# Kernel optimization log

Hardware: AMD Instinct MI355X
Metric: run time of the kernel (lower is better)

Reference implementation:

```python
import jax, jax.numpy as jnp
import numpy as np
import math

Ds = 2048
N = 16384
M = 1024


def setup_inputs() -> dict:
    key = jax.random.key(0)
    kD, kS, kW = jax.random.split(key, 3)
    D = jax.random.normal(kD, (N, Ds), dtype=jnp.float32)
    S = jax.random.normal(kS, (M, Ds), dtype=jnp.float32)
    W = jax.random.normal(kW, (Ds, Ds), dtype=jnp.float32) * 0.01  # init.normal std=0.01
    return {"D": D, "S": S, "W": W}


def reference(D, S, W):
    ds = D.shape[1]
    temperature = 1.0
    # cross-attention: [n, m]
    scores = (D @ S.T) / (math.sqrt(ds) * temperature)
    att_weight = jax.nn.softmax(scores, axis=1)
    att_S = att_weight @ S  # [n, Ds]
    # bilinear per row: logits[i] = D[i] . (W @ att_S[i])  -> fused einsum
    logits = jnp.einsum('nd,de,ne->n', D, W, att_S)
    log_prob = jnp.sum(jax.nn.log_sigmoid(logits))
    return log_prob
```

## Files before the change

kernel.cpp:

```cpp
#include <hip/hip_runtime.h>
#include <stdint.h>

typedef unsigned short u16;
typedef unsigned int u32;
typedef __attribute__((ext_vector_type(8))) short bf16x8;
typedef __attribute__((ext_vector_type(4))) float f32x4;

#define DS 2048
#define NROWS 16384
#define MS 1024
#define K2 2048

__device__ __forceinline__ u16 f2bf(float f) {
  u32 u = __float_as_uint(f);
  u32 r = (u + 0x7fffu + ((u >> 16) & 1u)) >> 16;
  return (u16)r;
}
__device__ __forceinline__ float bf2f(u16 h) {
  return __uint_as_float(((u32)h) << 16);
}

__global__ __launch_bounds__(256) void k_conv(const float* __restrict__ in,
                                              u16* __restrict__ out, int n4) {
  int i = blockIdx.x * blockDim.x + threadIdx.x;
  int stride = gridDim.x * blockDim.x;
  for (; i < n4; i += stride) {
    float4 v = ((const float4*)in)[i];
    ushort4 o;
    o.x = f2bf(v.x); o.y = f2bf(v.y); o.z = f2bf(v.z); o.w = f2bf(v.w);
    ((ushort4*)out)[i] = o;
  }
}

__global__ __launch_bounds__(256) void k_conv_S(const float* __restrict__ in,
                                                u16* __restrict__ Sbf,
                                                u16* __restrict__ Bt, int n4) {
  int i = blockIdx.x * blockDim.x + threadIdx.x;
  int stride = gridDim.x * blockDim.x;
  for (; i < n4; i += stride) {
    float4 v = ((const float4*)in)[i];
    ushort4 o;
    o.x = f2bf(v.x); o.y = f2bf(v.y); o.z = f2bf(v.z); o.w = f2bf(v.w);
    ((ushort4*)Sbf)[i] = o;
    int m = i >> 9;
    int c4 = i & 511;
    ((ushort4*)Bt)[(size_t)m * 1024 + c4] = o;
  }
}

__device__ __forceinline__ void gload16(const u16* g, u16* l) {
  __builtin_amdgcn_global_load_lds(
      (const __attribute__((address_space(1))) void*)g,
      (__attribute__((address_space(3))) void*)l, 16, 0, 0);
}

__global__ __launch_bounds__(256, 2) void k_gemm_bt64(const u16* __restrict__ A,
                                                      const u16* __restrict__ Bt,
                                                      u16* __restrict__ C, int ldc,
                                                      int K) {
  __shared__ u16 lsA[64 * 32];
  __shared__ u16 lsB[128 * 32];
  const int tid = threadIdx.x;
  const int wid = tid >> 6;
  const int lane = tid & 63;
  const int brow = blockIdx.y * 64;
  const int bcol = blockIdx.x * 128;
  const int wm = wid >> 1;
  const int wn = wid & 1;

  f32x4 acc[2][4];
#pragma unroll
  for (int i = 0; i < 2; ++i)
#pragma unroll
    for (int j = 0; j < 4; ++j) acc[i][j] = (f32x4){0.f, 0.f, 0.f, 0.f};

  const int srow = lane >> 2;
  const int skoct = (lane & 3) * 8;
  const u16* gA = A + (size_t)(brow + wid * 16 + srow) * K + skoct;
  const u16* gB = Bt + (size_t)(bcol + wid * 32 + srow) * K + skoct;
  u16* lA = &lsA[(wid * 16) * 32];
  u16* lB0 = &lsB[(wid * 32) * 32];
  u16* lB1 = &lsB[(wid * 32 + 16) * 32];
  const size_t row16 = (size_t)16 * K;

  const int arow = wm * 32 + (lane & 15);
  const int bcr = wn * 64 + (lane & 15);
  const int koff = (lane >> 4) * 8;

  for (int kt = 0; kt < K; kt += 32) {
    gload16(gA + kt, lA);
    gload16(gB + kt, lB0);
    gload16(gB + kt + row16, lB1);
    __syncthreads();
    bf16x8 af[2], bfr[4];
#pragma unroll
    for (int i = 0; i < 2; ++i) af[i] = *(const bf16x8*)&lsA[(arow + i * 16) * 32 + koff];
#pragma unroll
    for (int i = 0; i < 4; ++i) bfr[i] = *(const bf16x8*)&lsB[(bcr + i * 16) * 32 + koff];
#pragma unroll
    for (int mi = 0; mi < 2; ++mi)
#pragma unroll
      for (int ni = 0; ni < 4; ++ni)
        acc[mi][ni] = __builtin_amdgcn_mfma_f32_16x16x32_bf16(af[mi], bfr[ni],
                                                              acc[mi][ni], 0, 0, 0);
    __syncthreads();
  }

  const int crow0 = brow + wm * 32 + (lane >> 4) * 4;
  const int ccol0 = bcol + wn * 64 + (lane & 15);
#pragma unroll
  for (int mi = 0; mi < 2; ++mi)
#pragma unroll
    for (int ni = 0; ni < 4; ++ni)
#pragma unroll
      for (int r = 0; r < 4; ++r)
        C[(size_t)(crow0 + mi * 16 + r) * ldc + (ccol0 + ni * 16)] = f2bf(acc[mi][ni][r]);
}

#define SINV 0.022097086912079608f

#define DSR(d, a, IMM) \
  asm volatile("ds_read_b128 %0, %1 offset:%c2" : "=v"(d) : "v"(a), "n"(IMM))

#define RD_A0(k0, k1, dst)                              \
  DSR(dst[0][0], k0, 0);     DSR(dst[0][1], k1, 0);     \
  DSR(dst[1][0], k0, 2048);  DSR(dst[1][1], k1, 2048);  \
  DSR(dst[2][0], k0, 4096);  DSR(dst[2][1], k1, 4096);  \
  DSR(dst[3][0], k0, 6144);  DSR(dst[3][1], k1, 6144)
#define RD_A1(k0, k1, dst)                              \
  DSR(dst[0][0], k0, 16384); DSR(dst[0][1], k1, 16384); \
  DSR(dst[1][0], k0, 18432); DSR(dst[1][1], k1, 18432); \
  DSR(dst[2][0], k0, 20480); DSR(dst[2][1], k1, 20480); \
  DSR(dst[3][0], k0, 22528); DSR(dst[3][1], k1, 22528)
#define RD_B0(k0, k1, dst)                              \
  DSR(dst[0][0], k0, 0);     DSR(dst[0][1], k1, 0);     \
  DSR(dst[1][0], k0, 2048);  DSR(dst[1][1], k1, 2048)
#define RD_B1(k0, k1, dst)                              \
  DSR(dst[0][0], k0, 16384); DSR(dst[0][1], k1, 16384); \
  DSR(dst[1][0], k0, 18432); DSR(dst[1][1], k1, 18432)

#define MMAQ(AF, BQ, QM, QN)                                                       \
  do {                                                                             \
    _Pragma("unroll") for (int mi = 0; mi < 4; ++mi)                               \
        _Pragma("unroll") for (int ni = 0; ni < 2; ++ni) {                         \
      acc[QM][QN][mi][ni] = __builtin_amdgcn_mfma_f32_16x16x32_bf16(               \
          AF[mi][0], BQ[ni][0], acc[QM][QN][mi][ni], 0, 0, 0);                     \
      acc[QM][QN][mi][ni] = __builtin_amdgcn_mfma_f32_16x16x32_bf16(               \
          AF[mi][1], BQ[ni][1], acc[QM][QN][mi][ni], 0, 0, 0);                     \
    }                                                                              \
  } while (0)

#define LGKM(N)                                              \
  asm volatile("s_waitcnt lgkmcnt(" #N ")" ::: "memory");    \
  __builtin_amdgcn_sched_barrier(0)
#define VMW(N) asm volatile("s_waitcnt vmcnt(" #N ")" ::: "memory")
#define PRIO1() __builtin_amdgcn_s_setprio(1)
#define PRIO0() __builtin_amdgcn_s_setprio(0)
#define BAR() __builtin_amdgcn_s_barrier()

#define STGA(b, h, kt)                                                            \
  do {                                                                            \
    gload16(pA + (size_t)((h) * 128) * K2 + (kt),                                 \
            &lds[(b) * 32768 + (h) * 8192 + wid * 512]);                          \
    gload16(pA + (size_t)((h) * 128 + 64) * K2 + (kt),                            \
            &lds[(b) * 32768 + (h) * 8192 + 4096 + wid * 512]);                   \
  } while (0)
#define STGB(b, h, kt)                                                            \
  do {                                                                            \
    gload16(pB + (size_t)((h) * 128) * K2 + (kt),                                 \
            &lds[(b) * 32768 + 16384 + (h) * 8192 + wid * 512]);                  \
    gload16(pB + (size_t)((h) * 128 + 64) * K2 + (kt),                            \
            &lds[(b) * 32768 + 16384 + (h) * 8192 + 4096 + wid * 512]);           \
  } while (0)

__global__ __launch_bounds__(512, 2) void k_gemm8(const u16* __restrict__ A,
                                                  const u16* __restrict__ Bt,
                                                  float* __restrict__ Pnd) {
  extern __shared__ u16 lds[];
  const int tid = threadIdx.x;
  const int wid = tid >> 6;
  const int lane = tid & 63;
  const int bid = blockIdx.x;
  const int swz = (bid & 7) * 64 + (bid >> 3);
  const int by = swz >> 3, bx = swz & 7;
  const int brow = by * 256, bcol = bx * 256;
  const int wm = wid >> 2, wn = wid & 3;
  const int l15 = lane & 15, s0 = lane >> 4;

  const int tr = tid >> 3;
  const int scol = ((tid & 7) ^ (tr & 7)) << 3;
  const u16* pA = A + (size_t)(brow + tr) * K2 + scol;
  const u16* pB = Bt + (size_t)(bcol + tr) * K2 + scol;

  const u32 lb = (u32)(uintptr_t)(&lds[0]);
  const u32 xorp = ((u32)(s0 ^ (lane & 7))) << 4;
  const u32 aA00 = lb + ((u32)(wm * 64 + l15) << 7) + xorp;
  const u32 aA01 = aA00 ^ 64u;
  const u32 aA10 = aA00 + 65536u;
  const u32 aA11 = aA10 ^ 64u;
  const u32 aB00 = lb + 32768u + ((u32)(wn * 32 + l15) << 7) + xorp;
  const u32 aB01 = aB00 ^ 64u;
  const u32 aB10 = aB00 + 65536u;
  const u32 aB11 = aB10 ^ 64u;

  f32x4 acc[2][2][4][2];
#pragma unroll
  for (int a = 0; a < 2; ++a)
#pragma unroll
    for (int b = 0; b < 2; ++b)
#pragma unroll
      for (int c = 0; c < 4; ++c)
#pragma unroll
        for (int d = 0; d < 2; ++d) acc[a][b][c][d] = (f32x4){0.f, 0.f, 0.f, 0.f};

  bf16x8 afA[4][2], afB[4][2], bq0[2][2], bq1[2][2];

  STGA(0, 0, 0); STGB(0, 0, 0); STGB(0, 1, 0); STGA(0, 1, 0);
  STGA(1, 0, 64);
  VMW(2);
  BAR();
  RD_A0(aA00, aA01, afA);
  RD_B0(aB00, aB01, bq0);

  int kb = 0;
#pragma unroll 1
  for (int j = 0; j < 15; ++j, kb += 128) {
    STGB(1, 0, kb + 64);
    RD_B1(aB00, aB01, bq1);
    LGKM(4); PRIO1(); MMAQ(afA, bq0, 0, 0); PRIO0(); VMW(4); BAR();
    STGB(1, 1, kb + 64);
    RD_A1(aA00, aA01, afB);
    LGKM(8); PRIO1(); MMAQ(afA, bq1, 0, 1); PRIO0(); VMW(4); BAR();
    STGA(1, 1, kb + 64);
    LGKM(0); PRIO1(); MMAQ(afB, bq0, 1, 0); PRIO0(); VMW(4); BAR();
    STGA(0, 0, kb + 128);
    RD_A0(aA10, aA11, afA);
    RD_B0(aB10, aB11, bq0);
    LGKM(12); PRIO1(); MMAQ(afB, bq1, 1, 1); PRIO0(); VMW(4); BAR();
    STGB(0, 0, kb + 128);
    RD_B1(aB10, aB11, bq1);
    LGKM(4); PRIO1(); MMAQ(afA, bq0, 0, 0); PRIO0(); VMW(4); BAR();
    STGB(0, 1, kb + 128);
    RD_A1(aA10, aA11, afB);
    LGKM(8); PRIO1(); MMAQ(afA, bq1, 0, 1); PRIO0(); VMW(4); BAR();
    STGA(0, 1, kb + 128);
    LGKM(0); PRIO1(); MMAQ(afB, bq0, 1, 0); PRIO0(); VMW(4); BAR();
    STGA(1, 0, kb + 192);
    RD_A0(aA00, aA01, afA);
    RD_B0(aB00, aB01, bq0);
    LGKM(12); PRIO1(); MMAQ(afB, bq1, 1, 1); PRIO0(); VMW(4); BAR();
  }
  {
    STGB(1, 0, kb + 64);
    RD_B1(aB00, aB01, bq1);
    LGKM(4); PRIO1(); MMAQ(afA, bq0, 0, 0); PRIO0(); VMW(4); BAR();
    STGB(1, 1, kb + 64);
    RD_A1(aA00, aA01, afB);
    LGKM(8); PRIO1(); MMAQ(afA, bq1, 0, 1); PRIO0(); VMW(4); BAR();
    STGA(1, 1, kb + 64);
    LGKM(0); PRIO1(); MMAQ(afB, bq0, 1, 0); PRIO0(); VMW(4); BAR();
    RD_A0(aA10, aA11, afA);
    RD_B0(aB10, aB11, bq0);
    LGKM(12); PRIO1(); MMAQ(afB, bq1, 1, 1); PRIO0(); VMW(2); BAR();
    RD_B1(aB10, aB11, bq1);
    LGKM(4); PRIO1(); MMAQ(afA, bq0, 0, 0); PRIO0(); VMW(0); BAR();
    RD_A1(aA10, aA11, afB);
    LGKM(8); PRIO1(); MMAQ(afA, bq1, 0, 1); PRIO0();
    LGKM(0); PRIO1(); MMAQ(afB, bq0, 1, 0); PRIO0();
    MMAQ(afB, bq1, 1, 1);
  }

  __syncthreads();
  float* red = (float*)&lds[0];

#pragma unroll
  for (int qm = 0; qm < 2; ++qm)
#pragma unroll
    for (int mi = 0; mi < 4; ++mi)
#pragma unroll
      for (int r = 0; r < 4; ++r) {
        float num = 0.f, den = 0.f;
#pragma unroll
        for (int qn = 0; qn < 2; ++qn)
#pragma unroll
          for (int ni = 0; ni < 2; ++ni) {
            float v = acc[qm][qn][mi][ni][r];
            float g = __shfl_xor(v, 1);
            float e = __expf(v * SINV);
            num += e * g;
            den += e;
          }
        num += __shfl_xor(num, 2); den += __shfl_xor(den, 2);
        num += __shfl_xor(num, 4); den += __shfl_xor(den, 4);
        num += __shfl_xor(num, 8); den += __shfl_xor(den, 8);
        if (l15 == 0) {
          int slot = qm * 16 + mi * 4 + r;
          red[((wid * 32 + slot) * 4 + s0) * 2 + 0] = num;
          red[((wid * 32 + slot) * 4 + s0) * 2 + 1] = den;
        }
      }
  __syncthreads();
  {
    int rloc = tid >> 1, which = tid & 1;
    int qm = rloc >> 7, wmr = (rloc >> 6) & 1, mi = (rloc >> 4) & 3;
    int lg = (rloc >> 2) & 3, r = rloc & 3;
    int slot = qm * 16 + mi * 4 + r;
    float v = 0.f;
#pragma unroll
    for (int w2 = 0; w2 < 4; ++w2)
      v += red[(((wmr * 4 + w2) * 32 + slot) * 4 + lg) * 2 + which];
    Pnd[((size_t)(brow + rloc) * 8 + bx) * 2 + which] = v;
  }
}

__global__ __launch_bounds__(256) void k_rowfinal(const float* __restrict__ Pnd,
                                                  float* __restrict__ part) {
  int row = blockIdx.x * 256 + threadIdx.x;
  const float4* p = (const float4*)(Pnd + (size_t)row * 16);
  float num = 0.f, den = 0.f;
#pragma unroll
  for (int i = 0; i < 4; ++i) {
    float4 v = p[i];
    num += v.x + v.z;
    den += v.y + v.w;
  }
  float logit = num / den;
  float ls = (logit >= 0.f) ? -log1pf(__expf(-logit))
                            : (logit - log1pf(__expf(logit)));
  __shared__ float red[4];
#pragma unroll
  for (int off = 32; off > 0; off >>= 1) ls += __shfl_down(ls, off);
  if ((threadIdx.x & 63) == 0) red[threadIdx.x >> 6] = ls;
  __syncthreads();
  if (threadIdx.x == 0) part[blockIdx.x] = red[0] + red[1] + red[2] + red[3];
}

__global__ __launch_bounds__(64) void k_final64(const float* __restrict__ part,
                                                float* __restrict__ out) {
  float v = part[threadIdx.x];
#pragma unroll
  for (int off = 32; off > 0; off >>= 1) v += __shfl_down(v, off);
  if (threadIdx.x == 0) out[0] = v;
}

extern "C" void kernel_launch(void* const* d_in, const int* in_sizes, int n_in,
                              void* d_out, int out_size, void* d_ws, size_t ws_size,
                              hipStream_t stream) {
  const float* D = (const float*)d_in[0];
  const float* S = (const float*)d_in[1];
  const float* W = (const float*)d_in[2];

  char* w = (char*)d_ws;
  u16* Dbf = (u16*)w; w += (size_t)NROWS * DS * 2;
  u16* Bt = (u16*)w;  w += (size_t)DS * DS * 2;
  u16* Wbf = (u16*)w; w += (size_t)DS * DS * 2;
  u16* Sbf = (u16*)w; w += (size_t)MS * DS * 2;
  float* Pnd = (float*)w; w += (size_t)NROWS * 16 * 4;
  float* part = (float*)w;

  (void)hipFuncSetAttribute((const void*)k_gemm8,
                            hipFuncAttributeMaxDynamicSharedMemorySize, 131072);

  k_conv<<<1024, 256, 0, stream>>>(W, Wbf, DS * DS / 4);
  k_conv_S<<<512, 256, 0, stream>>>(S, Sbf, Bt, MS * DS / 4);
  k_conv<<<2048, 256, 0, stream>>>(D, Dbf, NROWS * DS / 4);

  k_gemm_bt64<<<dim3(DS / 128, MS / 64), 256, 0, stream>>>(
      Sbf, Wbf, Bt + DS, 2 * DS, DS);

  k_gemm8<<<512, 512, 131072, stream>>>(Dbf, Bt, Pnd);

  k_rowfinal<<<NROWS / 256, 256, 0, stream>>>(Pnd, part);
  k_final64<<<1, 64, 0, stream>>>(part, (float*)d_out);
}
```

Measured before the change: 188.7 us.

## Fuse conversions and S·W gemm into one pre-kernel loading fp32 directly

Replaces three conversion kernels and the small bf16 S×W gemm with a single launch. The first 256 blocks run the S×W gemm straight from fp32 inputs. They stage tiles into swizzled, double-buffered LDS with global_load_lds, convert to bf16 in registers with v_cvt_pk_bf16_f32, and issue MFMAs. The remaining blocks convert D and S to bf16. This removes the Wbf and Sbf intermediate buffers and several launches, and lets the gemm overlap with the D conversion. The cost is twice the LDS traffic per tile and a mixed-role grid.

```diff
diff --git a/kernel.cpp b/kernel.cpp
--- a/kernel.cpp
+++ b/kernel.cpp
@@ -5,6 +5,7 @@
 typedef unsigned int u32;
 typedef __attribute__((ext_vector_type(8))) short bf16x8;
 typedef __attribute__((ext_vector_type(4))) float f32x4;
+typedef __attribute__((ext_vector_type(4))) u32 u32x4;
 
 #define DS 2048
 #define NROWS 16384
@@ -16,37 +17,6 @@
   u32 r = (u + 0x7fffu + ((u >> 16) & 1u)) >> 16;
   return (u16)r;
 }
-__device__ __forceinline__ float bf2f(u16 h) {
-  return __uint_as_float(((u32)h) << 16);
-}
-
-__global__ __launch_bounds__(256) void k_conv(const float* __restrict__ in,
-                                              u16* __restrict__ out, int n4) {
-  int i = blockIdx.x * blockDim.x + threadIdx.x;
-  int stride = gridDim.x * blockDim.x;
-  for (; i < n4; i += stride) {
-    float4 v = ((const float4*)in)[i];
-    ushort4 o;
-    o.x = f2bf(v.x); o.y = f2bf(v.y); o.z = f2bf(v.z); o.w = f2bf(v.w);
-    ((ushort4*)out)[i] = o;
-  }
-}
-
-__global__ __launch_bounds__(256) void k_conv_S(const float* __restrict__ in,
-                                                u16* __restrict__ Sbf,
-                                                u16* __restrict__ Bt, int n4) {
-  int i = blockIdx.x * blockDim.x + threadIdx.x;
-  int stride = gridDim.x * blockDim.x;
-  for (; i < n4; i += stride) {
-    float4 v = ((const float4*)in)[i];
-    ushort4 o;
-    o.x = f2bf(v.x); o.y = f2bf(v.y); o.z = f2bf(v.z); o.w = f2bf(v.w);
-    ((ushort4*)Sbf)[i] = o;
-    int m = i >> 9;
-    int c4 = i & 511;
-    ((ushort4*)Bt)[(size_t)m * 1024 + c4] = o;
-  }
-}
 
 __device__ __forceinline__ void gload16(const u16* g, u16* l) {
   __builtin_amdgcn_global_load_lds(
@@ -54,19 +24,80 @@
       (__attribute__((address_space(3))) void*)l, 16, 0, 0);
 }
 
-__global__ __launch_bounds__(256, 2) void k_gemm_bt64(const u16* __restrict__ A,
-                                                      const u16* __restrict__ Bt,
-                                                      u16* __restrict__ C, int ldc,
-                                                      int K) {
-  __shared__ u16 lsA[64 * 32];
-  __shared__ u16 lsB[128 * 32];
+#define DSR(d, a, IMM) \
+  asm volatile("ds_read_b128 %0, %1 offset:%c2" : "=v"(d) : "v"(a), "n"(IMM))
+#define CVTPK(d, lo, hi) \
+  asm("v_cvt_pk_bf16_f32 %0, %1, %2" : "=v"(d) : "v"(lo), "v"(hi))
+#define LGKM(N)                                              \
+  asm volatile("s_waitcnt lgkmcnt(" #N ")" ::: "memory");    \
+  __builtin_amdgcn_sched_barrier(0)
+#define VMW(N) asm volatile("s_waitcnt vmcnt(" #N ")" ::: "memory")
+#define SB0() __builtin_amdgcn_sched_barrier(0)
+#define PRIO1() __builtin_amdgcn_s_setprio(1)
+#define PRIO0() __builtin_amdgcn_s_setprio(0)
+#define BAR() __builtin_amdgcn_s_barrier()
+
+#define CVT8(dst, lo, hi)                                         \
+  do {                                                            \
+    u32 _c0, _c1, _c2, _c3;                                       \
+    CVTPK(_c0, lo[0], lo[1]); CVTPK(_c1, lo[2], lo[3]);           \
+    CVTPK(_c2, hi[0], hi[1]); CVTPK(_c3, hi[2], hi[3]);           \
+    u32x4 _q = {_c0, _c1, _c2, _c3};                              \
+    dst = *(bf16x8*)&_q;                                          \
+  } while (0)
+
+__global__ __launch_bounds__(256) void k_pre(const float* __restrict__ D,
+                                             const float* __restrict__ S,
+                                             const float* __restrict__ W,
+                                             u16* __restrict__ Dbf,
+                                             u16* __restrict__ Bt) {
+  __shared__ float lsA[2][64 * 32];
+  __shared__ float lsB[2][128 * 32];
+  const int bid = blockIdx.x;
   const int tid = threadIdx.x;
-  const int wid = tid >> 6;
-  const int lane = tid & 63;
-  const int brow = blockIdx.y * 64;
-  const int bcol = blockIdx.x * 128;
-  const int wm = wid >> 1;
-  const int wn = wid & 1;
+
+  if (bid >= 256) {
+    if (bid < 2304) {
+      size_t i = (size_t)(bid - 256) * 256 + tid;
+#pragma unroll
+      for (int it = 0; it < 16; ++it, i += (size_t)2048 * 256) {
+        float4 v = ((const float4*)D)[i];
+        ushort4 o;
+        o.x = f2bf(v.x); o.y = f2bf(v.y); o.z = f2bf(v.z); o.w = f2bf(v.w);
+        ((ushort4*)Dbf)[i] = o;
+      }
+    } else {
+      size_t j = (size_t)(bid - 2304) * 256 + tid;
+#pragma unroll
+      for (int it = 0; it < 16; ++it, j += (size_t)128 * 256) {
+        float4 v = ((const float4*)S)[j];
+        ushort4 o;
+        o.x = f2bf(v.x); o.y = f2bf(v.y); o.z = f2bf(v.z); o.w = f2bf(v.w);
+        int m = (int)(j >> 9), c4 = (int)(j & 511);
+        ((ushort4*)Bt)[(size_t)m * 1024 + c4] = o;
+      }
+    }
+    return;
+  }
+
+  const int wid = tid >> 6, lane = tid & 63;
+  const int brow = (bid >> 4) * 64;
+  const int bcol = (bid & 15) * 128;
+  const int wm = wid >> 1, wn = wid & 1;
+  const int l15 = lane & 15, s0 = lane >> 4;
+
+  const int sr = tid >> 3;
+  const int soct = (tid & 7) ^ (sr & 7);
+  const float* gS = S + (size_t)(brow + sr) * 2048 + soct * 4;
+  const float* gW = W + (size_t)(bcol + sr) * 2048 + soct * 4;
+
+  const u32 lbA = (u32)(uintptr_t)&lsA[0][0];
+  const u32 lbB = (u32)(uintptr_t)&lsB[0][0];
+  const u32 swz = (u32)(((2 * s0) ^ (l15 & 7)) * 16);
+  const u32 aA = lbA + (u32)(wm * 32 + l15) * 128 + swz;
+  const u32 aAx = aA ^ 16u;
+  const u32 aB = lbB + (u32)(wn * 64 + l15) * 128 + swz;
+  const u32 aBx = aB ^ 16u;
 
   f32x4 acc[2][4];
 #pragma unroll
@@ -74,53 +105,67 @@
 #pragma unroll
     for (int j = 0; j < 4; ++j) acc[i][j] = (f32x4){0.f, 0.f, 0.f, 0.f};
 
-  const int srow = lane >> 2;
-  const int skoct = (lane & 3) * 8;
-  const u16* gA = A + (size_t)(brow + wid * 16 + srow) * K + skoct;
-  const u16* gB = Bt + (size_t)(bcol + wid * 32 + srow) * K + skoct;
-  u16* lA = &lsA[(wid * 16) * 32];
-  u16* lB0 = &lsB[(wid * 32) * 32];
-  u16* lB1 = &lsB[(wid * 32 + 16) * 32];
-  const size_t row16 = (size_t)16 * K;
-
-  const int arow = wm * 32 + (lane & 15);
-  const int bcr = wn * 64 + (lane & 15);
-  const int koff = (lane >> 4) * 8;
-
-  for (int kt = 0; kt < K; kt += 32) {
-    gload16(gA + kt, lA);
-    gload16(gB + kt, lB0);
-    gload16(gB + kt + row16, lB1);
-    __syncthreads();
+#define VSTG(b, kt)                                                              \
+  do {                                                                           \
+    gload16((const u16*)(gS + (kt)),             (u16*)(&lsA[b][0] + wid * 256)); \
+    gload16((const u16*)(gS + 32 * 2048 + (kt)), (u16*)(&lsA[b][1024] + wid * 256)); \
+    gload16((const u16*)(gW + (kt)),             (u16*)(&lsB[b][0] + wid * 256)); \
+    gload16((const u16*)(gW + 32 * 2048 + (kt)), (u16*)(&lsB[b][1024] + wid * 256)); \
+    gload16((const u16*)(gW + 64 * 2048 + (kt)), (u16*)(&lsB[b][2048] + wid * 256)); \
+    gload16((const u16*)(gW + 96 * 2048 + (kt)), (u16*)(&lsB[b][3072] + wid * 256)); \
+  } while (0)
+
+  VSTG(0, 0);
+#pragma unroll 1
+  for (int t = 0; t < 64; ++t) {
+    const int b = t & 1;
+    const u32 oA = (u32)(b * 8192), oB = (u32)(b * 16384);
+    if (t < 63) {
+      VSTG(b ^ 1, (t + 1) * 32);
+      VMW(6);
+    } else {
+      VMW(0);
+    }
+    BAR(); SB0();
+    f32x4 qa0, qa1, qa2, qa3;
+    f32x4 qb0, qb1, qb2, qb3, qb4, qb5, qb6, qb7;
+    DSR(qa0, aA + oA, 0);     DSR(qa1, aAx + oA, 0);
+    DSR(qa2, aA + oA, 2048);  DSR(qa3, aAx + oA, 2048);
+    DSR(qb0, aB + oB, 0);     DSR(qb1, aBx + oB, 0);
+    DSR(qb2, aB + oB, 2048);  DSR(qb3, aBx + oB, 2048);
+    DSR(qb4, aB + oB, 4096);  DSR(qb5, aBx + oB, 4096);
+    DSR(qb6, aB + oB, 6144);  DSR(qb7, aBx + oB, 6144);
+    LGKM(0);
     bf16x8 af[2], bfr[4];
-#pragma unroll
-    for (int i = 0; i < 2; ++i) af[i] = *(const bf16x8*)&lsA[(arow + i * 16) * 32 + koff];
-#pragma unroll
-    for (int i = 0; i < 4; ++i) bfr[i] = *(const bf16x8*)&lsB[(bcr + i * 16) * 32 + koff];
+    CVT8(af[0], qa0, qa1); CVT8(af[1], qa2, qa3);
+    CVT8(bfr[0], qb0, qb1); CVT8(bfr[1], qb2, qb3);
+    CVT8(bfr[2], qb4, qb5); CVT8(bfr[3], qb6, qb7);
+    PRIO1();
 #pragma unroll
     for (int mi = 0; mi < 2; ++mi)
 #pragma unroll
       for (int ni = 0; ni < 4; ++ni)
         acc[mi][ni] = __builtin_amdgcn_mfma_f32_16x16x32_bf16(af[mi], bfr[ni],
                                                               acc[mi][ni], 0, 0, 0);
-    __syncthreads();
-  }
-
-  const int crow0 = brow + wm * 32 + (lane >> 4) * 4;
-  const int ccol0 = bcol + wn * 64 + (lane & 15);
+    PRIO0(); SB0();
+    BAR();
+  }
+#undef VSTG
+
+  const int crow0 = brow + wm * 32 + s0 * 4;
+  const int ccol0 = bcol + wn * 64 + l15;
+  u16* C = Bt + 2048;
 #pragma unroll
   for (int mi = 0; mi < 2; ++mi)
 #pragma unroll
     for (int ni = 0; ni < 4; ++ni)
 #pragma unroll
       for (int r = 0; r < 4; ++r)
-        C[(size_t)(crow0 + mi * 16 + r) * ldc + (ccol0 + ni * 16)] = f2bf(acc[mi][ni][r]);
+        C[(size_t)(crow0 + mi * 16 + r) * 4096 + (ccol0 + ni * 16)] =
+            f2bf(acc[mi][ni][r]);
 }
 
 #define SINV 0.022097086912079608f
-
-#define DSR(d, a, IMM) \
-  asm volatile("ds_read_b128 %0, %1 offset:%c2" : "=v"(d) : "v"(a), "n"(IMM))
 
 #define RD_A0(k0, k1, dst)                              \
   DSR(dst[0][0], k0, 0);     DSR(dst[0][1], k1, 0);     \
@@ -149,14 +194,6 @@
           AF[mi][1], BQ[ni][1], acc[QM][QN][mi][ni], 0, 0, 0);                     \
     }                                                                              \
   } while (0)
-
-#define LGKM(N)                                              \
-  asm volatile("s_waitcnt lgkmcnt(" #N ")" ::: "memory");    \
-  __builtin_amdgcn_sched_barrier(0)
-#define VMW(N) asm volatile("s_waitcnt vmcnt(" #N ")" ::: "memory")
-#define PRIO1() __builtin_amdgcn_s_setprio(1)
-#define PRIO0() __builtin_amdgcn_s_setprio(0)
-#define BAR() __builtin_amdgcn_s_barrier()
 
 #define STGA(b, h, kt)                                                            \
   do {                                                                            \
@@ -353,20 +390,13 @@
   char* w = (char*)d_ws;
   u16* Dbf = (u16*)w; w += (size_t)NROWS * DS * 2;
   u16* Bt = (u16*)w;  w += (size_t)DS * DS * 2;
-  u16* Wbf = (u16*)w; w += (size_t)DS * DS * 2;
-  u16* Sbf = (u16*)w; w += (size_t)MS * DS * 2;
   float* Pnd = (float*)w; w += (size_t)NROWS * 16 * 4;
   float* part = (float*)w;
 
   (void)hipFuncSetAttribute((const void*)k_gemm8,
                             hipFuncAttributeMaxDynamicSharedMemorySize, 131072);
 
-  k_conv<<<1024, 256, 0, stream>>>(W, Wbf, DS * DS / 4);
-  k_conv_S<<<512, 256, 0, stream>>>(S, Sbf, Bt, MS * DS / 4);
-  k_conv<<<2048, 256, 0, stream>>>(D, Dbf, NROWS * DS / 4);
-
-  k_gemm_bt64<<<dim3(DS / 128, MS / 64), 256, 0, stream>>>(
-      Sbf, Wbf, Bt + DS, 2 * DS, DS);
+  k_pre<<<2432, 256, 0, stream>>>(D, S, W, Dbf, Bt);
 
   k_gemm8<<<512, 512, 131072, stream>>>(Dbf, Bt, Pnd);
 
```

New measurement: 169.8 us. -10.1%, faster.
